# Optimization experiments

Measured on AMD Instinct MI355X. Metric: run time of the kernel, lower is better.

The kernel has to match this reference:

```python
import jax, jax.numpy as jnp
import numpy as np

N = 262144   # nodes
E = 4194304  # edges (avg degree 16)
G = 1024     # graphs in batch
F_IN, F_GCN, F_DENSE = 3, 16, 16
NEG_SLOPE = 0.01  # nn.LeakyReLU default


def _leaky(x):
    return jax.nn.leaky_relu(x, NEG_SLOPE)


def _gcn_conv(x, W, b, src, dst, ew):
    """PyG GCNConv: h = x @ W; symmetric deg-norm with self-loops (weight 1);
    out[i] = sum_{(j->i)} norm_e * h[j] + (1/deg_i) * h[i] + b."""
    h = x @ W                                   # [N, out]
    deg = jax.ops.segment_sum(ew, dst, num_segments=N) + 1.0  # +1 from self-loop
    dinv = jnp.where(deg > 0, jax.lax.rsqrt(deg), 0.0)        # deg^{-1/2}
    norm = dinv[src] * ew * dinv[dst]           # [E]
    agg = jax.ops.segment_sum(h[src] * norm[:, None], dst, num_segments=N)
    agg = agg + h * (dinv * dinv)[:, None]      # self-loop message, norm = 1/deg
    return agg + b


def setup_inputs() -> dict:
    key = jax.random.key(0)
    ks = jax.random.split(key, 24)
    inp = {
        "X": jax.random.normal(ks[0], (N, F_IN), dtype=jnp.float32),
        "Edge_index": jax.random.randint(ks[1], (2, E), 0, N, dtype=jnp.int64) if jax.config.jax_enable_x64 else jax.random.randint(ks[1], (2, E), 0, N, dtype=jnp.int32),
        "Edge_weight": jax.random.uniform(ks[2], (E,), dtype=jnp.float32),
        "Batching": jnp.sort(jax.random.randint(ks[3], (N,), 0, G, dtype=jnp.int32)),
        "num_graphs": G,
    }
    def lin(k, fi, fo):
        kw, kb = jax.random.split(k)
        s = 1.0 / np.sqrt(fi)
        return (jax.random.uniform(kw, (fi, fo), minval=-s, maxval=s, dtype=jnp.float32),
                jax.random.uniform(kb, (fo,), minval=-s, maxval=s, dtype=jnp.float32))
    inp["W1"], inp["b1"] = lin(ks[4], F_IN, F_GCN)
    inp["W2"], inp["b2"] = lin(ks[5], F_GCN, F_GCN)
    inp["Wp1"], inp["bp1"] = lin(ks[6], F_GCN, F_DENSE)
    inp["Wp2"], inp["bp2"] = lin(ks[7], F_DENSE, F_DENSE)
    inp["Wp3"], inp["bp3"] = lin(ks[8], F_DENSE, 2)
    inp["Wt1"], inp["bt1"] = lin(ks[9], F_GCN, F_DENSE)
    inp["Wt2"], inp["bt2"] = lin(ks[10], F_DENSE, F_DENSE)
    inp["Wt3"], inp["bt3"] = lin(ks[11], F_DENSE, 2)
    return inp


def reference(X, Edge_index, Edge_weight, Batching, num_graphs,
              W1, b1, W2, b2,
              Wp1, bp1, Wp2, bp2, Wp3, bp3,
              Wt1, bt1, Wt2, bt2, Wt3, bt3):
    src, dst = Edge_index[0], Edge_index[1]
    out = _leaky(_gcn_conv(X, W1, b1, src, dst, Edge_weight))
    out = _leaky(_gcn_conv(out, W2, b2, src, dst, Edge_weight))
    # global mean pool over graphs
    sums = jax.ops.segment_sum(out, Batching, num_segments=num_graphs)
    cnt = jax.ops.segment_sum(jnp.ones((out.shape[0],), out.dtype), Batching,
                              num_segments=num_graphs)
    pooled = sums / jnp.maximum(cnt, 1.0)[:, None]   # [G, 16]
    Phi = _leaky(pooled @ Wp1 + bp1)
    Phi = _leaky(Phi @ Wp2 + bp2)
    Phi = Phi @ Wp3 + bp3
    Theta = _leaky(pooled @ Wt1 + bt1)
    Theta = _leaky(Theta @ Wt2 + bt2)
    Theta = Theta @ Wt3 + bt3
    return jnp.concatenate((Phi, Theta), axis=1)   # [G, 4]
```

## Files before the change

kernel.cpp:

```cpp
#include <hip/hip_runtime.h>


#define NBUCK 512
#define BCAP  10240
#define CHUNK 8192
#define APT   16
#define NTILE 8
#define TSH   15
#define RCAP  20

__device__ __forceinline__ float leaky(float x) { return x > 0.f ? x : 0.01f * x; }

__global__ __launch_bounds__(512) void
binA_kernel(const int* __restrict__ src, const int* __restrict__ dst,
            const float* __restrict__ ew, int* __restrict__ bucketCursor,
            int2* __restrict__ coarse, int E) {
    __shared__ int lhist[NBUCK], lbase[NBUCK], lcur[NBUCK], gbase[NBUCK];
    __shared__ int tmp[NBUCK];
    __shared__ int2 stag[CHUNK];
    __shared__ unsigned short sbuck[CHUNK];
    int t = threadIdx.x;
    int base = blockIdx.x * CHUNK;
    lhist[t] = 0; lcur[t] = 0;
    __syncthreads();
    int n = min(CHUNK, E - base);
    int myDst[APT], mySrc[APT]; float myEw[APT];
#pragma unroll
    for (int k = 0; k < APT; ++k) {
        int j = t + k * 512;
        if (j < n) {
            int d = dst[base + j];
            myDst[k] = d; mySrc[k] = src[base + j]; myEw[k] = ew[base + j];
            atomicAdd(&lhist[d >> 9], 1);
        } else myDst[k] = -1;
    }
    __syncthreads();
    int hv = lhist[t];
    tmp[t] = hv;
    __syncthreads();
    for (int off = 1; off < NBUCK; off <<= 1) {
        int v = (t >= off) ? tmp[t - off] : 0;
        __syncthreads();
        tmp[t] += v;
        __syncthreads();
    }
    lbase[t] = tmp[t] - hv;
    gbase[t] = hv ? atomicAdd(&bucketCursor[t], hv) : 0;
    __syncthreads();
#pragma unroll
    for (int k = 0; k < APT; ++k) {
        int d = myDst[k];
        if (d >= 0) {
            int b = d >> 9;
            int p = lbase[b] + atomicAdd(&lcur[b], 1);
            stag[p] = make_int2(mySrc[k] | ((d & 511) << 18), __float_as_int(myEw[k]));
            sbuck[p] = (unsigned short)b;
        }
    }
    __syncthreads();
    for (int j = t; j < n; j += 512) {
        int b = sbuck[j];
        coarse[(size_t)b * BCAP + gbase[b] + (j - lbase[b])] = stag[j];
    }
}

__global__ void bscan_kernel(const int* __restrict__ bucketCursor,
                             int* __restrict__ bucketBase, int* __restrict__ row,
                             int N, int E) {
    __shared__ int s[NBUCK];
    int t = threadIdx.x;
    int v = bucketCursor[t];
    s[t] = v;
    __syncthreads();
    for (int off = 1; off < NBUCK; off <<= 1) {
        int x = (t >= off) ? s[t - off] : 0;
        __syncthreads();
        s[t] += x;
        __syncthreads();
    }
    bucketBase[t] = s[t] - v;
    if (t == 0) row[N] = E;
}

__global__ __launch_bounds__(512, 2) void
binB_kernel(const int* __restrict__ bucketCursor, const int* __restrict__ bucketBase,
            const int2* __restrict__ coarse, int2* __restrict__ edata,
            int* __restrict__ row, float* __restrict__ dinv,
            uint4* __restrict__ tcnt) {
    __shared__ int2 sedata[BCAP];
    __shared__ int loff[NBUCK * NTILE];
    __shared__ int tmp[512];
    int b = blockIdx.x, t = threadIdx.x;
    for (int i = t; i < NBUCK * NTILE; i += 512) loff[i] = 0;
    __syncthreads();
    int cnt = bucketCursor[b];
    int gb  = bucketBase[b];
    const int2* cb = coarse + (size_t)b * BCAP;
    int2 myE[RCAP]; int myKey[RCAP];
#pragma unroll
    for (int k = 0; k < RCAP; ++k) {
        int j = t + k * 512;
        if (j < cnt) {
            int2 e = cb[j];
            myE[k] = e;
            myKey[k] = (((e.x >> 18) & 511) << 3) | ((e.x & 0x3FFFF) >> TSH);
            atomicAdd(&loff[myKey[k]], 1);
        } else myKey[k] = -1;
    }
    __syncthreads();
    int base8 = t * 8, s = 0;
#pragma unroll
    for (int k = 0; k < 8; ++k) s += loff[base8 + k];
    tmp[t] = s;
    __syncthreads();
    for (int off = 1; off < 512; off <<= 1) {
        int v = (t >= off) ? tmp[t - off] : 0;
        __syncthreads();
        tmp[t] += v;
        __syncthreads();
    }
    int run = tmp[t] - s;
    int o[9];
#pragma unroll
    for (int k = 0; k < 8; ++k) { int v = loff[base8 + k]; o[k] = run; loff[base8 + k] = run; run += v; }
    o[8] = run;
    __syncthreads();
    int node = b * 512 + t;
    row[node] = gb + o[0];
    uint4 p;
    p.x = (unsigned)(o[1] - o[0]) | ((unsigned)(o[2] - o[1]) << 16);
    p.y = (unsigned)(o[3] - o[2]) | ((unsigned)(o[4] - o[3]) << 16);
    p.z = (unsigned)(o[5] - o[4]) | ((unsigned)(o[6] - o[5]) << 16);
    p.w = (unsigned)(o[7] - o[6]) | ((unsigned)(o[8] - o[7]) << 16);
    tcnt[node] = p;
#pragma unroll
    for (int k = 0; k < RCAP; ++k) {
        if (myKey[k] >= 0) {
            int pos = atomicAdd(&loff[myKey[k]], 1);
            sedata[pos] = make_int2(myE[k].x & 0x3FFFF, myE[k].y);
        }
    }
    __syncthreads();
    for (int j = t; j < cnt; j += 512) edata[gb + j] = sedata[j];
    float dsum = 0.f;
    for (int j = o[0]; j < o[8]; ++j) dsum += __int_as_float(sedata[j].y);
    dinv[node] = rsqrtf(1.0f + dsum);
}

__global__ void pack_kernel(const float* __restrict__ X, const float* __restrict__ dinv,
                            float4* __restrict__ Xp, int N) {
    int i = blockIdx.x * blockDim.x + threadIdx.x;
    if (i >= N) return;
    Xp[i] = make_float4(X[3 * i], X[3 * i + 1], X[3 * i + 2], dinv[i]);
}

__global__ __launch_bounds__(512) void
aggA_kernel(const int* __restrict__ row, const uint4* __restrict__ tcnt,
            const int2* __restrict__ edata, const float4* __restrict__ Xp,
            const float* __restrict__ W1, const float* __restrict__ b1,
            const float* __restrict__ W2, float* __restrict__ h2) {
    __shared__ float w1s[48];
    __shared__ float w[256];
    __shared__ float bb[16];
    __shared__ float sx[128][17];
    int t = threadIdx.x;
    if (t < 256) w[t] = W2[t];
    else if (t < 272) bb[t - 256] = b1[t - 256];
    else if (t >= 288 && t < 336) w1s[t - 288] = W1[t - 288];
    __syncthreads();
    int ln = t >> 2, l = t & 3;
    float w1r0[4], w1r1[4], w1r2[4];
#pragma unroll
    for (int c = 0; c < 4; ++c) {
        w1r0[c] = w1s[0 * 16 + 4 * l + c];
        w1r1[c] = w1s[1 * 16 + 4 * l + c];
        w1r2[c] = w1s[2 * 16 + 4 * l + c];
    }
    int iA = blockIdx.x * 256 + ln, iB = iA + 128;
    int eA = row[iA], eB = row[iB];
    uint4 cAv = tcnt[iA], cBv = tcnt[iB];
    unsigned ca[4] = {cAv.x, cAv.y, cAv.z, cAv.w};
    unsigned cb[4] = {cBv.x, cBv.y, cBv.z, cBv.w};
    float4 xpA = Xp[iA], xpB = Xp[iB];
    float diA = xpA.w, diB = xpB.w;
    float accA[4], accB[4];
#pragma unroll
    for (int c = 0; c < 4; ++c) {
        accA[c] = (xpA.x * w1r0[c] + xpA.y * w1r1[c] + xpA.z * w1r2[c]) * diA;
        accB[c] = (xpB.x * w1r0[c] + xpB.y * w1r1[c] + xpB.z * w1r2[c]) * diB;
    }
#pragma unroll
    for (int tt = 0; tt < NTILE; ++tt) {
        int nA = (ca[tt >> 1] >> ((tt & 1) * 16)) & 0xFFFF;
        int nB = (cb[tt >> 1] >> ((tt & 1) * 16)) & 0xFFFF;
        for (int e = eA + nA; eA < e; ++eA) {
            int2 ed = edata[eA];
            float4 xs = Xp[ed.x];
            float f = __int_as_float(ed.y) * xs.w;
            float f0 = xs.x * f, f1 = xs.y * f, f2 = xs.z * f;
#pragma unroll
            for (int c = 0; c < 4; ++c)
                accA[c] += f0 * w1r0[c] + f1 * w1r1[c] + f2 * w1r2[c];
        }
        for (int e = eB + nB; eB < e; ++eB) {
            int2 ed = edata[eB];
            float4 xs = Xp[ed.x];
            float f = __int_as_float(ed.y) * xs.w;
            float f0 = xs.x * f, f1 = xs.y * f, f2 = xs.z * f;
#pragma unroll
            for (int c = 0; c < 4; ++c)
                accB[c] += f0 * w1r0[c] + f1 * w1r1[c] + f2 * w1r2[c];
        }
        __syncthreads();
    }
    sx[ln][4 * l + 0] = leaky(diA * accA[0] + bb[4 * l + 0]);
    sx[ln][4 * l + 1] = leaky(diA * accA[1] + bb[4 * l + 1]);
    sx[ln][4 * l + 2] = leaky(diA * accA[2] + bb[4 * l + 2]);
    sx[ln][4 * l + 3] = leaky(diA * accA[3] + bb[4 * l + 3]);
    __syncthreads();
    {
        float a0 = 0.f, a1 = 0.f, a2 = 0.f, a3 = 0.f;
#pragma unroll
        for (int q = 0; q < 16; ++q) {
            float xv = sx[ln][q];
            a0 += xv * w[q * 16 + 4 * l + 0];
            a1 += xv * w[q * 16 + 4 * l + 1];
            a2 += xv * w[q * 16 + 4 * l + 2];
            a3 += xv * w[q * 16 + 4 * l + 3];
        }
        ((float4*)h2)[(size_t)iA * 4 + l] = make_float4(a0 * diA, a1 * diA, a2 * diA, a3 * diA);
    }
    __syncthreads();
    sx[ln][4 * l + 0] = leaky(diB * accB[0] + bb[4 * l + 0]);
    sx[ln][4 * l + 1] = leaky(diB * accB[1] + bb[4 * l + 1]);
    sx[ln][4 * l + 2] = leaky(diB * accB[2] + bb[4 * l + 2]);
    sx[ln][4 * l + 3] = leaky(diB * accB[3] + bb[4 * l + 3]);
    __syncthreads();
    {
        float a0 = 0.f, a1 = 0.f, a2 = 0.f, a3 = 0.f;
#pragma unroll
        for (int q = 0; q < 16; ++q) {
            float xv = sx[ln][q];
            a0 += xv * w[q * 16 + 4 * l + 0];
            a1 += xv * w[q * 16 + 4 * l + 1];
            a2 += xv * w[q * 16 + 4 * l + 2];
            a3 += xv * w[q * 16 + 4 * l + 3];
        }
        ((float4*)h2)[(size_t)iB * 4 + l] = make_float4(a0 * diB, a1 * diB, a2 * diB, a3 * diB);
    }
}

__global__ __launch_bounds__(512) void
aggB_kernel(const int* __restrict__ row, const uint4* __restrict__ tcnt,
            const int2* __restrict__ edata, const float* __restrict__ dinv,
            const float* __restrict__ h2prime, float* __restrict__ agg2) {
    int t = threadIdx.x;
    int ln = t >> 2, l = t & 3;
    int iA = blockIdx.x * 256 + ln, iB = iA + 128;
    const float4* hp = (const float4*)h2prime;
    int eA = row[iA], eB = row[iB];
    uint4 cAv = tcnt[iA], cBv = tcnt[iB];
    unsigned ca[4] = {cAv.x, cAv.y, cAv.z, cAv.w};
    unsigned cb[4] = {cBv.x, cBv.y, cBv.z, cBv.w};
    float diA = dinv[iA], diB = dinv[iB];
    float4 accA = hp[(size_t)iA * 4 + l];
    float4 accB = hp[(size_t)iB * 4 + l];
#pragma unroll
    for (int tt = 0; tt < NTILE; ++tt) {
        int nA = (ca[tt >> 1] >> ((tt & 1) * 16)) & 0xFFFF;
        int nB = (cb[tt >> 1] >> ((tt & 1) * 16)) & 0xFFFF;
        for (int e = eA + nA; eA < e; ++eA) {
            int2 ed = edata[eA];
            float ewv = __int_as_float(ed.y);
            float4 v = hp[(size_t)ed.x * 4 + l];
            accA.x += v.x * ewv; accA.y += v.y * ewv;
            accA.z += v.z * ewv; accA.w += v.w * ewv;
        }
        for (int e = eB + nB; eB < e; ++eB) {
            int2 ed = edata[eB];
            float ewv = __int_as_float(ed.y);
            float4 v = hp[(size_t)ed.x * 4 + l];
            accB.x += v.x * ewv; accB.y += v.y * ewv;
            accB.z += v.z * ewv; accB.w += v.w * ewv;
        }
        __syncthreads();
    }
    ((float4*)agg2)[(size_t)iA * 4 + l] =
        make_float4(accA.x * diA, accA.y * diA, accA.z * diA, accA.w * diA);
    ((float4*)agg2)[(size_t)iB * 4 + l] =
        make_float4(accB.x * diB, accB.y * diB, accB.z * diB, accB.w * diB);
}

__device__ void head_mlp(const float* pooled,
                         const float* __restrict__ Wa, const float* __restrict__ ba,
                         const float* __restrict__ Wb, const float* __restrict__ bb,
                         const float* __restrict__ Wc, const float* __restrict__ bc,
                         float* o) {
    float t[16], u[16];
#pragma unroll
    for (int f = 0; f < 16; ++f) {
        float a = ba[f];
        for (int k = 0; k < 16; ++k) a += pooled[k] * Wa[k * 16 + f];
        t[f] = leaky(a);
    }
#pragma unroll
    for (int f = 0; f < 16; ++f) {
        float a = bb[f];
        for (int k = 0; k < 16; ++k) a += t[k] * Wb[k * 16 + f];
        u[f] = leaky(a);
    }
    float o0 = bc[0], o1 = bc[1];
    for (int k = 0; k < 16; ++k) { o0 += u[k] * Wc[2 * k]; o1 += u[k] * Wc[2 * k + 1]; }
    o[0] = o0; o[1] = o1;
}

__global__ void pool_head_kernel(const float* __restrict__ agg2, const float* __restrict__ b2,
                                 const int* __restrict__ batching, int N,
                                 const float* __restrict__ Wp1, const float* __restrict__ bp1,
                                 const float* __restrict__ Wp2, const float* __restrict__ bp2,
                                 const float* __restrict__ Wp3, const float* __restrict__ bp3,
                                 const float* __restrict__ Wt1, const float* __restrict__ bt1,
                                 const float* __restrict__ Wt2, const float* __restrict__ bt2,
                                 const float* __restrict__ Wt3, const float* __restrict__ bt3,
                                 float* __restrict__ out) {
    int g = blockIdx.x;
    __shared__ int bounds[2];
    if (threadIdx.x < 2) {
        int v = g + (int)threadIdx.x;
        int lo = 0, hi = N;
        while (lo < hi) { int m = (lo + hi) >> 1; if (batching[m] < v) lo = m + 1; else hi = m; }
        bounds[threadIdx.x] = lo;
    }
    __syncthreads();
    int lo = bounds[0], hi = bounds[1];
    int f = threadIdx.x & 15, r = threadIdx.x >> 4;
    float bf = b2[f];
    float acc = 0.f;
    for (int i = lo + r; i < hi; i += 16) acc += leaky(agg2[(size_t)i * 16 + f] + bf);
    __shared__ float red[16][17];
    red[r][f] = acc;
    __syncthreads();
    __shared__ float pooled[16];
    if (r == 0) {
        float s = 0.f;
#pragma unroll
        for (int k = 0; k < 16; ++k) s += red[k][f];
        pooled[f] = s / fmaxf((float)(hi - lo), 1.0f);
    }
    __syncthreads();
    if (threadIdx.x == 0) {
        float o[2];
        head_mlp(pooled, Wp1, bp1, Wp2, bp2, Wp3, bp3, o);
        out[4 * g + 0] = o[0]; out[4 * g + 1] = o[1];
    } else if (threadIdx.x == 1) {
        float o[2];
        head_mlp(pooled, Wt1, bt1, Wt2, bt2, Wt3, bt3, o);
        out[4 * g + 2] = o[0]; out[4 * g + 3] = o[1];
    }
}

extern "C" void kernel_launch(void* const* d_in, const int* in_sizes, int n_in,
                              void* d_out, int out_size, void* d_ws, size_t ws_size,
                              hipStream_t stream) {
    const float* X        = (const float*)d_in[0];
    const int*   ei       = (const int*)d_in[1];
    const float* ew       = (const float*)d_in[2];
    const int*   batching = (const int*)d_in[3];
    const float* W1  = (const float*)d_in[5];  const float* b1  = (const float*)d_in[6];
    const float* W2  = (const float*)d_in[7];  const float* b2  = (const float*)d_in[8];
    const float* Wp1 = (const float*)d_in[9];  const float* bp1 = (const float*)d_in[10];
    const float* Wp2 = (const float*)d_in[11]; const float* bp2 = (const float*)d_in[12];
    const float* Wp3 = (const float*)d_in[13]; const float* bp3 = (const float*)d_in[14];
    const float* Wt1 = (const float*)d_in[15]; const float* bt1 = (const float*)d_in[16];
    const float* Wt2 = (const float*)d_in[17]; const float* bt2 = (const float*)d_in[18];
    const float* Wt3 = (const float*)d_in[19]; const float* bt3 = (const float*)d_in[20];

    const int N = in_sizes[3];
    const int E = in_sizes[2];
    const int G = out_size / 4;
    const int* src = ei;
    const int* dst = ei + E;

    char* ws = (char*)d_ws;
    size_t off = 0;
    int2*  edata = (int2*)(ws + off);  off += (size_t)E * 8;
    char*  regionA = ws + off;         off += (size_t)N * 64 * 3;
    int2*  coarse = (int2*)regionA;
    float* h2     = (float*)regionA;
    float* agg2   = (float*)(regionA + (size_t)N * 64);
    float4* Xp    = (float4*)(regionA + (size_t)N * 128);
    int*   bucketCursor = (int*)(ws + off); off += NBUCK * 4;
    int*   bucketBase   = (int*)(ws + off); off += NBUCK * 4;
    int*   row   = (int*)(ws + off);   off += (size_t)(N + 4) * 4;
    float* dinv  = (float*)(ws + off); off += (size_t)N * 4;
    uint4* tcnt  = (uint4*)(ws + off); off += (size_t)N * 16;
    float* out   = (float*)d_out;

    hipMemsetAsync(bucketCursor, 0, NBUCK * 4, stream);

    const int tb = 256;
    binA_kernel<<<(E + CHUNK - 1) / CHUNK, 512, 0, stream>>>(src, dst, ew, bucketCursor, coarse, E);
    bscan_kernel<<<1, NBUCK, 0, stream>>>(bucketCursor, bucketBase, row, N, E);
    binB_kernel<<<NBUCK, 512, 0, stream>>>(bucketCursor, bucketBase, coarse, edata, row, dinv, tcnt);
    pack_kernel<<<(N + tb - 1) / tb, tb, 0, stream>>>(X, dinv, Xp, N);
    aggA_kernel<<<N / 256, 512, 0, stream>>>(row, tcnt, edata, Xp, W1, b1, W2, h2);
    aggB_kernel<<<N / 256, 512, 0, stream>>>(row, tcnt, edata, dinv, h2, agg2);
    pool_head_kernel<<<G, tb, 0, stream>>>(agg2, b2, batching, N,
                                           Wp1, bp1, Wp2, bp2, Wp3, bp3,
                                           Wt1, bt1, Wt2, bt2, Wt3, bt3, out);
}
```

Baseline: 348.4 us.

## Sort bucket edges tile-major and stage per-tile edge segments in LDS

Bucket edges are now ordered by source tile first and destination node second, so each source tile's edges for a bucket sit in one contiguous segment. binB emits per-node tile offsets and per-bucket tile starts in place of a row pointer. The aggregation kernels cooperatively load each tile's half-segment into shared memory with coalesced reads, then read edges from LDS rather than doing per-thread strided global loads. This adds an extra metadata array and a sync per tile. It also assumes a half-segment fits in SEGCAP (1024) entries, which holds for the average case but is not guaranteed.

```diff
diff --git a/kernel.cpp b/kernel.cpp
--- a/kernel.cpp
+++ b/kernel.cpp
@@ -8,6 +8,7 @@
 #define NTILE 8
 #define TSH   15
 #define RCAP  20
+#define SEGCAP 1024
 
 __device__ __forceinline__ float leaky(float x) { return x > 0.f ? x : 0.01f * x; }
 
@@ -65,8 +66,7 @@
 }
 
 __global__ void bscan_kernel(const int* __restrict__ bucketCursor,
-                             int* __restrict__ bucketBase, int* __restrict__ row,
-                             int N, int E) {
+                             int* __restrict__ bucketBase) {
     __shared__ int s[NBUCK];
     int t = threadIdx.x;
     int v = bucketCursor[t];
@@ -79,17 +79,17 @@
         __syncthreads();
     }
     bucketBase[t] = s[t] - v;
-    if (t == 0) row[N] = E;
 }
 
 __global__ __launch_bounds__(512, 2) void
 binB_kernel(const int* __restrict__ bucketCursor, const int* __restrict__ bucketBase,
             const int2* __restrict__ coarse, int2* __restrict__ edata,
-            int* __restrict__ row, float* __restrict__ dinv,
-            uint4* __restrict__ tcnt) {
+            float* __restrict__ dinv, uint4* __restrict__ tcnt,
+            uint4* __restrict__ ntoff, int* __restrict__ tstartAbs) {
     __shared__ int2 sedata[BCAP];
     __shared__ int loff[NBUCK * NTILE];
     __shared__ int tmp[512];
+    __shared__ int tbase[NTILE + 1];
     int b = blockIdx.x, t = threadIdx.x;
     for (int i = t; i < NBUCK * NTILE; i += 512) loff[i] = 0;
     __syncthreads();
@@ -103,7 +103,8 @@
         if (j < cnt) {
             int2 e = cb[j];
             myE[k] = e;
-            myKey[k] = (((e.x >> 18) & 511) << 3) | ((e.x & 0x3FFFF) >> TSH);
+            int sv = e.x & 0x3FFFF;
+            myKey[k] = ((sv >> TSH) << 9) | ((e.x >> 18) & 511);
             atomicAdd(&loff[myKey[k]], 1);
         } else myKey[k] = -1;
     }
@@ -120,19 +121,34 @@
         __syncthreads();
     }
     int run = tmp[t] - s;
-    int o[9];
-#pragma unroll
-    for (int k = 0; k < 8; ++k) { int v = loff[base8 + k]; o[k] = run; loff[base8 + k] = run; run += v; }
-    o[8] = run;
-    __syncthreads();
+#pragma unroll
+    for (int k = 0; k < 8; ++k) { int v = loff[base8 + k]; loff[base8 + k] = run; run += v; }
+    __syncthreads();
+    if (t < 8) tbase[t] = loff[t * 512];
+    if (t == 0) tbase[8] = cnt;
+    __syncthreads();
+    int o[8], c[8];
+#pragma unroll
+    for (int tt = 0; tt < 8; ++tt) {
+        int cur = loff[tt * 512 + t];
+        int nxt = (t < 511) ? loff[tt * 512 + t + 1] : tbase[tt + 1];
+        o[tt] = cur - tbase[tt];
+        c[tt] = nxt - cur;
+    }
     int node = b * 512 + t;
-    row[node] = gb + o[0];
-    uint4 p;
-    p.x = (unsigned)(o[1] - o[0]) | ((unsigned)(o[2] - o[1]) << 16);
-    p.y = (unsigned)(o[3] - o[2]) | ((unsigned)(o[4] - o[3]) << 16);
-    p.z = (unsigned)(o[5] - o[4]) | ((unsigned)(o[6] - o[5]) << 16);
-    p.w = (unsigned)(o[7] - o[6]) | ((unsigned)(o[8] - o[7]) << 16);
+    uint4 p, q;
+    p.x = (unsigned)c[0] | ((unsigned)c[1] << 16);
+    p.y = (unsigned)c[2] | ((unsigned)c[3] << 16);
+    p.z = (unsigned)c[4] | ((unsigned)c[5] << 16);
+    p.w = (unsigned)c[6] | ((unsigned)c[7] << 16);
     tcnt[node] = p;
+    q.x = (unsigned)o[0] | ((unsigned)o[1] << 16);
+    q.y = (unsigned)o[2] | ((unsigned)o[3] << 16);
+    q.z = (unsigned)o[4] | ((unsigned)o[5] << 16);
+    q.w = (unsigned)o[6] | ((unsigned)o[7] << 16);
+    ntoff[node] = q;
+    if (t < 9) tstartAbs[b * 9 + t] = gb + tbase[t];
+    __syncthreads();
 #pragma unroll
     for (int k = 0; k < RCAP; ++k) {
         if (myKey[k] >= 0) {
@@ -143,7 +159,11 @@
     __syncthreads();
     for (int j = t; j < cnt; j += 512) edata[gb + j] = sedata[j];
     float dsum = 0.f;
-    for (int j = o[0]; j < o[8]; ++j) dsum += __int_as_float(sedata[j].y);
+#pragma unroll
+    for (int tt = 0; tt < 8; ++tt) {
+        int s0 = tbase[tt] + o[tt];
+        for (int k = 0; k < c[tt]; ++k) dsum += __int_as_float(sedata[s0 + k].y);
+    }
     dinv[node] = rsqrtf(1.0f + dsum);
 }
 
@@ -155,10 +175,12 @@
 }
 
 __global__ __launch_bounds__(512) void
-aggA_kernel(const int* __restrict__ row, const uint4* __restrict__ tcnt,
-            const int2* __restrict__ edata, const float4* __restrict__ Xp,
-            const float* __restrict__ W1, const float* __restrict__ b1,
-            const float* __restrict__ W2, float* __restrict__ h2) {
+aggA_kernel(const int* __restrict__ tstartAbs, const uint4* __restrict__ tcnt,
+            const uint4* __restrict__ ntoff, const int2* __restrict__ edata,
+            const float4* __restrict__ Xp, const float* __restrict__ W1,
+            const float* __restrict__ b1, const float* __restrict__ W2,
+            float* __restrict__ h2) {
+    __shared__ int2 sedge[SEGCAP];
     __shared__ float w1s[48];
     __shared__ float w[256];
     __shared__ float bb[16];
@@ -176,11 +198,19 @@
         w1r1[c] = w1s[1 * 16 + 4 * l + c];
         w1r2[c] = w1s[2 * 16 + 4 * l + c];
     }
+    int bk = blockIdx.x >> 1, half = blockIdx.x & 1;
     int iA = blockIdx.x * 256 + ln, iB = iA + 128;
-    int eA = row[iA], eB = row[iB];
+    int tsr[9];
+#pragma unroll
+    for (int k = 0; k < 9; ++k) tsr[k] = tstartAbs[bk * 9 + k];
     uint4 cAv = tcnt[iA], cBv = tcnt[iB];
+    uint4 oAv = ntoff[iA], oBv = ntoff[iB];
+    uint4 mV  = ntoff[bk * 512 + 256];
     unsigned ca[4] = {cAv.x, cAv.y, cAv.z, cAv.w};
-    unsigned cb[4] = {cBv.x, cBv.y, cBv.z, cBv.w};
+    unsigned cbv[4] = {cBv.x, cBv.y, cBv.z, cBv.w};
+    unsigned oa[4] = {oAv.x, oAv.y, oAv.z, oAv.w};
+    unsigned ob[4] = {oBv.x, oBv.y, oBv.z, oBv.w};
+    unsigned mr[4] = {mV.x, mV.y, mV.z, mV.w};
     float4 xpA = Xp[iA], xpB = Xp[iB];
     float diA = xpA.w, diB = xpB.w;
     float accA[4], accB[4];
@@ -191,21 +221,30 @@
     }
 #pragma unroll
     for (int tt = 0; tt < NTILE; ++tt) {
+        int midRel = (mr[tt >> 1] >> ((tt & 1) * 16)) & 0xFFFF;
+        int segBase = tsr[tt];
+        int ls = segBase + (half ? midRel : 0);
+        int le = half ? tsr[tt + 1] : segBase + midRel;
+        for (int j = ls + t; j < le; j += 512) sedge[j - ls] = edata[j];
+        __syncthreads();
+        int rel = half ? midRel : 0;
+        int sA = (int)((oa[tt >> 1] >> ((tt & 1) * 16)) & 0xFFFF) - rel;
         int nA = (ca[tt >> 1] >> ((tt & 1) * 16)) & 0xFFFF;
-        int nB = (cb[tt >> 1] >> ((tt & 1) * 16)) & 0xFFFF;
-        for (int e = eA + nA; eA < e; ++eA) {
-            int2 ed = edata[eA];
-            float4 xs = Xp[ed.x];
-            float f = __int_as_float(ed.y) * xs.w;
+        for (int k = 0; k < nA; ++k) {
+            int2 e = sedge[sA + k];
+            float4 xs = Xp[e.x];
+            float f = __int_as_float(e.y) * xs.w;
             float f0 = xs.x * f, f1 = xs.y * f, f2 = xs.z * f;
 #pragma unroll
             for (int c = 0; c < 4; ++c)
                 accA[c] += f0 * w1r0[c] + f1 * w1r1[c] + f2 * w1r2[c];
         }
-        for (int e = eB + nB; eB < e; ++eB) {
-            int2 ed = edata[eB];
-            float4 xs = Xp[ed.x];
-            float f = __int_as_float(ed.y) * xs.w;
+        int sB = (int)((ob[tt >> 1] >> ((tt & 1) * 16)) & 0xFFFF) - rel;
+        int nB = (cbv[tt >> 1] >> ((tt & 1) * 16)) & 0xFFFF;
+        for (int k = 0; k < nB; ++k) {
+            int2 e = sedge[sB + k];
+            float4 xs = Xp[e.x];
+            float f = __int_as_float(e.y) * xs.w;
             float f0 = xs.x * f, f1 = xs.y * f, f2 = xs.z * f;
 #pragma unroll
             for (int c = 0; c < 4; ++c)
@@ -251,35 +290,54 @@
 }
 
 __global__ __launch_bounds__(512) void
-aggB_kernel(const int* __restrict__ row, const uint4* __restrict__ tcnt,
-            const int2* __restrict__ edata, const float* __restrict__ dinv,
-            const float* __restrict__ h2prime, float* __restrict__ agg2) {
+aggB_kernel(const int* __restrict__ tstartAbs, const uint4* __restrict__ tcnt,
+            const uint4* __restrict__ ntoff, const int2* __restrict__ edata,
+            const float* __restrict__ dinv, const float* __restrict__ h2prime,
+            float* __restrict__ agg2) {
+    __shared__ int2 sedge[SEGCAP];
     int t = threadIdx.x;
     int ln = t >> 2, l = t & 3;
+    int bk = blockIdx.x >> 1, half = blockIdx.x & 1;
     int iA = blockIdx.x * 256 + ln, iB = iA + 128;
     const float4* hp = (const float4*)h2prime;
-    int eA = row[iA], eB = row[iB];
+    int tsr[9];
+#pragma unroll
+    for (int k = 0; k < 9; ++k) tsr[k] = tstartAbs[bk * 9 + k];
     uint4 cAv = tcnt[iA], cBv = tcnt[iB];
+    uint4 oAv = ntoff[iA], oBv = ntoff[iB];
+    uint4 mV  = ntoff[bk * 512 + 256];
     unsigned ca[4] = {cAv.x, cAv.y, cAv.z, cAv.w};
-    unsigned cb[4] = {cBv.x, cBv.y, cBv.z, cBv.w};
+    unsigned cbv[4] = {cBv.x, cBv.y, cBv.z, cBv.w};
+    unsigned oa[4] = {oAv.x, oAv.y, oAv.z, oAv.w};
+    unsigned ob[4] = {oBv.x, oBv.y, oBv.z, oBv.w};
+    unsigned mr[4] = {mV.x, mV.y, mV.z, mV.w};
     float diA = dinv[iA], diB = dinv[iB];
     float4 accA = hp[(size_t)iA * 4 + l];
     float4 accB = hp[(size_t)iB * 4 + l];
 #pragma unroll
     for (int tt = 0; tt < NTILE; ++tt) {
+        int midRel = (mr[tt >> 1] >> ((tt & 1) * 16)) & 0xFFFF;
+        int segBase = tsr[tt];
+        int ls = segBase + (half ? midRel : 0);
+        int le = half ? tsr[tt + 1] : segBase + midRel;
+        for (int j = ls + t; j < le; j += 512) sedge[j - ls] = edata[j];
+        __syncthreads();
+        int rel = half ? midRel : 0;
+        int sA = (int)((oa[tt >> 1] >> ((tt & 1) * 16)) & 0xFFFF) - rel;
         int nA = (ca[tt >> 1] >> ((tt & 1) * 16)) & 0xFFFF;
-        int nB = (cb[tt >> 1] >> ((tt & 1) * 16)) & 0xFFFF;
-        for (int e = eA + nA; eA < e; ++eA) {
-            int2 ed = edata[eA];
-            float ewv = __int_as_float(ed.y);
-            float4 v = hp[(size_t)ed.x * 4 + l];
+        for (int k = 0; k < nA; ++k) {
+            int2 e = sedge[sA + k];
+            float ewv = __int_as_float(e.y);
+            float4 v = hp[(size_t)e.x * 4 + l];
             accA.x += v.x * ewv; accA.y += v.y * ewv;
             accA.z += v.z * ewv; accA.w += v.w * ewv;
         }
-        for (int e = eB + nB; eB < e; ++eB) {
-            int2 ed = edata[eB];
-            float ewv = __int_as_float(ed.y);
-            float4 v = hp[(size_t)ed.x * 4 + l];
+        int sB = (int)((ob[tt >> 1] >> ((tt & 1) * 16)) & 0xFFFF) - rel;
+        int nB = (cbv[tt >> 1] >> ((tt & 1) * 16)) & 0xFFFF;
+        for (int k = 0; k < nB; ++k) {
+            int2 e = sedge[sB + k];
+            float ewv = __int_as_float(e.y);
+            float4 v = hp[(size_t)e.x * 4 + l];
             accB.x += v.x * ewv; accB.y += v.y * ewv;
             accB.z += v.z * ewv; accB.w += v.w * ewv;
         }
@@ -391,20 +449,22 @@
     float4* Xp    = (float4*)(regionA + (size_t)N * 128);
     int*   bucketCursor = (int*)(ws + off); off += NBUCK * 4;
     int*   bucketBase   = (int*)(ws + off); off += NBUCK * 4;
-    int*   row   = (int*)(ws + off);   off += (size_t)(N + 4) * 4;
     float* dinv  = (float*)(ws + off); off += (size_t)N * 4;
     uint4* tcnt  = (uint4*)(ws + off); off += (size_t)N * 16;
+    uint4* ntoff = (uint4*)(ws + off); off += (size_t)N * 16;
+    int*   tstartAbs = (int*)(ws + off); off += (size_t)NBUCK * 9 * 4;
     float* out   = (float*)d_out;
 
     hipMemsetAsync(bucketCursor, 0, NBUCK * 4, stream);
 
     const int tb = 256;
     binA_kernel<<<(E + CHUNK - 1) / CHUNK, 512, 0, stream>>>(src, dst, ew, bucketCursor, coarse, E);
-    bscan_kernel<<<1, NBUCK, 0, stream>>>(bucketCursor, bucketBase, row, N, E);
-    binB_kernel<<<NBUCK, 512, 0, stream>>>(bucketCursor, bucketBase, coarse, edata, row, dinv, tcnt);
+    bscan_kernel<<<1, NBUCK, 0, stream>>>(bucketCursor, bucketBase);
+    binB_kernel<<<NBUCK, 512, 0, stream>>>(bucketCursor, bucketBase, coarse, edata,
+                                           dinv, tcnt, ntoff, tstartAbs);
     pack_kernel<<<(N + tb - 1) / tb, tb, 0, stream>>>(X, dinv, Xp, N);
-    aggA_kernel<<<N / 256, 512, 0, stream>>>(row, tcnt, edata, Xp, W1, b1, W2, h2);
-    aggB_kernel<<<N / 256, 512, 0, stream>>>(row, tcnt, edata, dinv, h2, agg2);
+    aggA_kernel<<<N / 256, 512, 0, stream>>>(tstartAbs, tcnt, ntoff, edata, Xp, W1, b1, W2, h2);
+    aggB_kernel<<<N / 256, 512, 0, stream>>>(tstartAbs, tcnt, ntoff, edata, dinv, h2, agg2);
     pool_head_kernel<<<G, tb, 0, stream>>>(agg2, b2, batching, N,
                                            Wp1, bp1, Wp2, bp2, Wp3, bp3,
                                            Wt1, bt1, Wt2, bt2, Wt3, bt3, out);
```

New measurement: 396.6 us. +13.9%, slower.
